# Optimization experiments

Hardware: AMD Instinct MI355X
Metric: run time of the kernel (lower is better)

Reference implementation:

```python
import jax, jax.numpy as jnp
import numpy as np

B, N, D = 64, 256, 768
ITER_STEPS = 1


def _linear_w(key, out_d, in_d):
    s = 1.0 / np.sqrt(in_d)
    return jax.random.uniform(key, (out_d, in_d), jnp.float32, -s, s)


def setup_inputs() -> dict:
    key = jax.random.key(0)
    ks = jax.random.split(key, 16)
    node = jax.random.normal(ks[0], (B, N, D), jnp.float32)
    node_mask = jnp.ones((B, N), jnp.int32)
    argument_graph = jax.random.randint(ks[1], (B, N, N), 0, 2, jnp.int32)
    punctuation_graph = jax.random.randint(ks[2], (B, N, N), 0, 2, jnp.int32)
    inp = {
        "node": node,
        "node_mask": node_mask,
        "argument_graph": argument_graph,
        "punctuation_graph": punctuation_graph,
        # node-relatedness scorer: Linear(D, 1, bias=True)
        "Wq": _linear_w(ks[3], 1, D),
        "bq": jnp.zeros((1,), jnp.float32),
        # self node fc: Linear(D, D, bias=True)
        "Ws": _linear_w(ks[4], D, D),
        "bs": jnp.zeros((D,), jnp.float32),
        # 8 relation projections, Linear(D, D, bias=False)
        "Wa": _linear_w(ks[5], D, D),
        "Wp": _linear_w(ks[6], D, D),
        "Wap": _linear_w(ks[7], D, D),
        "Wpp": _linear_w(ks[8], D, D),
        "Wa2": _linear_w(ks[9], D, D),
        "Wp2": _linear_w(ks[10], D, D),
        "Wap2": _linear_w(ks[11], D, D),
        "Wpp2": _linear_w(ks[12], D, D),
    }
    return inp


def reference(node, node_mask, argument_graph, punctuation_graph,
              Wq, bq, Ws, bs, Wa, Wp, Wap, Wpp, Wa2, Wp2, Wap2, Wpp2):
    f32 = jnp.float32
    mask = node_mask.astype(f32)                      # [B, N]
    n = node.shape[1]
    eye = jnp.eye(n, dtype=f32)
    # dd_graph: node_mask outer product with zeroed diagonal
    dd = mask[:, None, :] * mask[:, :, None] * (1.0 - eye)   # [B, N, N]
    g_a = dd * argument_graph.astype(f32)
    g_p = dd * punctuation_graph.astype(f32)
    # reverse directed edges
    g_ar = dd * jnp.swapaxes(g_a, 1, 2)
    g_pr = dd * jnp.swapaxes(g_p, 1, 2)
    neigh = g_a.sum(-1) + g_p.sum(-1) + g_ar.sum(-1) + g_pr.sum(-1)  # [B, N]
    denom = jnp.where(neigh >= 1.0, neigh, 1.0)

    all_weight = []
    for _ in range(ITER_STEPS):
        # (1) node relatedness
        dw = jax.nn.sigmoid(jnp.einsum('bnd,od->bno', node, Wq) + bq)[..., 0]  # [B, N]
        all_weight.append(dw)
        self_info = jnp.einsum('bnd,ed->bne', node, Ws) + bs

        def msg(g, W):
            # node_weight: broadcast dw over rows, zero where no edge
            nw = dw[:, None, :] * g                    # [B, N, N]
            proj = jnp.einsum('bnd,ed->bne', node, W)  # [B, N, D]
            return jnp.matmul(nw, proj)                # [B, N, D]

        agg = (msg(g_a, Wa) + msg(g_p, Wp) + msg(g_ar, Wap) + msg(g_pr, Wpp)
               + msg(g_a, Wa2) + msg(g_p, Wp2) + msg(g_ar, Wap2) + msg(g_pr, Wpp2))
        agg = agg / denom[..., None]
        # (3) node update
        node = jax.nn.relu(self_info + agg)

    all_weight = jnp.stack(all_weight, axis=1)  # [B, steps, N]
    return node, all_weight
```

## Files before the change

kernel.cpp:

```cpp
#include <hip/hip_runtime.h>
#include <hip/hip_bf16.h>
#include <math.h>

typedef __bf16 bf16;
typedef unsigned char u8;
typedef unsigned long long ull;
typedef __bf16 bf16x8 __attribute__((ext_vector_type(8)));
typedef float f32x4 __attribute__((ext_vector_type(4)));

#define BB 64
#define NN 256
#define DD 768
#define MM (BB*NN)
#define KP 1024
#define WSZ (DD*DD)
#define TL2 272
#define AROW2 196608


__device__ __forceinline__ void async16(const void* g, void* l) {
  __builtin_amdgcn_global_load_lds((__attribute__((address_space(1))) void*)g,
                                   (__attribute__((address_space(3))) void*)l,
                                   16, 0, 0);
}

__device__ __forceinline__ void stage_tile(const bf16* gsrc, int ld, char* ldst,
                                           int wv, int lane) {
#pragma unroll
  for (int cc = 0; cc < 2; ++cc) {
    int c = wv * 2 + cc;
    int row = c * 16 + (lane >> 2);
    int col = (lane & 3) * 8;
    async16(gsrc + (size_t)row * ld + col, ldst + c * 1024);
  }
}

__device__ __forceinline__ void mma_step(const char* lA, const char* lB,
                                         f32x4 acc[4][4], int lane, int wr, int wc) {
  bf16x8 af[4], bfr[4];
  int rbase = wr * 64 + (lane & 15);
  int cbase = wc * 64 + (lane & 15);
  int ko = (lane >> 4) * 8;
#pragma unroll
  for (int r = 0; r < 4; ++r)
    af[r] = *(const bf16x8*)(lA + (((rbase + r * 16) * 32) + ko) * 2);
#pragma unroll
  for (int c = 0; c < 4; ++c)
    bfr[c] = *(const bf16x8*)(lB + (((cbase + c * 16) * 32) + ko) * 2);
#pragma unroll
  for (int r = 0; r < 4; ++r)
#pragma unroll
    for (int c = 0; c < 4; ++c)
      acc[r][c] = __builtin_amdgcn_mfma_f32_16x16x32_bf16(af[r], bfr[c], acc[r][c], 0, 0, 0);
}

__device__ __forceinline__ void mma_step_fp8t(const char* lA, const char* lB,
                                              f32x4 acc[4][4], int lane, int wr, int wc) {
  long af[4], bfr[4];
  int koq = (lane >> 4) * 1024;
  int mA = (wr * 64 + (lane & 15)) * 8;
  int mB = (wc * 64 + (lane & 15)) * 8;
#pragma unroll
  for (int r = 0; r < 4; ++r)
    af[r] = *(const long*)(lA + koq + mA + r * 128);
#pragma unroll
  for (int c = 0; c < 4; ++c)
    bfr[c] = *(const long*)(lB + koq + mB + c * 128);
#pragma unroll
  for (int r = 0; r < 4; ++r)
#pragma unroll
    for (int c = 0; c < 4; ++c)
      acc[r][c] = __builtin_amdgcn_mfma_f32_16x16x32_fp8_fp8(af[r], bfr[c], acc[r][c], 0, 0, 0);
}

__device__ __forceinline__ void k_step64(const bf16* Ab, int lda, const bf16* Bb, int ldb,
                                         char* smem, f32x4 acc[4][4],
                                         int wv, int lane, int wr, int wc) {
  char* lA0 = smem;
  char* lA1 = smem + 8192;
  char* lB0 = smem + 16384;
  char* lB1 = smem + 24576;
  __syncthreads();
  stage_tile(Ab, lda, lA0, wv, lane);
  stage_tile(Ab + 32, lda, lA1, wv, lane);
  stage_tile(Bb, ldb, lB0, wv, lane);
  stage_tile(Bb + 32, ldb, lB1, wv, lane);
  __builtin_amdgcn_s_waitcnt(0);
  __syncthreads();
  mma_step(lA0, lB0, acc, lane, wr, wc);
  mma_step(lA1, lB1, acc, lane, wr, wc);
}

__device__ __forceinline__ unsigned pack4(float a, float b, float c, float d) {
  int w = 0;
  w = __builtin_amdgcn_cvt_pk_fp8_f32(a, b, w, false);
  w = __builtin_amdgcn_cvt_pk_fp8_f32(c, d, w, true);
  return (unsigned)w;
}

__global__ void k_pre(const float* __restrict__ node, const float* __restrict__ Wq,
                      const float* __restrict__ bq, bf16* __restrict__ node_bf,
                      float* __restrict__ dw, float* __restrict__ allw,
                      float* __restrict__ neigh,
                      const float* __restrict__ Ws,
                      const float* __restrict__ Wa, const float* __restrict__ Wp,
                      const float* __restrict__ Wap, const float* __restrict__ Wpp,
                      const float* __restrict__ Wa2, const float* __restrict__ Wp2,
                      const float* __restrict__ Wap2, const float* __restrict__ Wpp2,
                      bf16* __restrict__ Wcat4, bf16* __restrict__ Ws_bf) {
  if (blockIdx.x < MM / 4) {
    int lane = threadIdx.x & 63, wv = threadIdx.x >> 6;
    int row = blockIdx.x * 4 + wv;
    const float* nr = node + (size_t)row * DD;
    bf16* nb = node_bf + (size_t)row * DD;
    float s = 0.f;
#pragma unroll
    for (int k = 0; k < DD / 64; ++k) {
      int idx = lane + k * 64;
      float v = nr[idx];
      nb[idx] = (bf16)v;
      s += v * Wq[idx];
    }
#pragma unroll
    for (int off = 32; off; off >>= 1) s += __shfl_down(s, off);
    if (lane == 0) {
      float z = s + bq[0];
      float d = 1.f / (1.f + expf(-z));
      dw[row] = d;
      allw[row] = d;
      neigh[row] = 0.f;
    }
  } else {
    int i = (blockIdx.x - MM / 4) * 256 + threadIdx.x;
    Ws_bf[i] = (bf16)Ws[i];
    Wcat4[i]           = (bf16)(Wa[i] + Wa2[i]);
    Wcat4[i + WSZ]     = (bf16)(Wp[i] + Wp2[i]);
    Wcat4[i + 2 * WSZ] = (bf16)(Wap[i] + Wap2[i]);
    Wcat4[i + 3 * WSZ] = (bf16)(Wpp[i] + Wpp2[i]);
  }
}

__device__ __forceinline__ void store_tiled(u8* base, int tile, int kin, int m, uint4 v) {
  size_t o = (size_t)tile * 4096 + (size_t)((kin >> 3) * 1024 + m * 8);
  *(ull*)(base + o)        = ((ull)v.y << 32) | v.x;
  *(ull*)(base + o + 1024) = ((ull)v.w << 32) | v.z;
}

__global__ void k_graph(const int* __restrict__ mask, const int* __restrict__ arg,
                        const int* __restrict__ pun, const float* __restrict__ dw,
                        u8* __restrict__ g8, float* __restrict__ neigh) {
  __shared__ float la[64][65];
  __shared__ float lp[64][65];
  __shared__ float msk[256];
  __shared__ float dwv[256];
  int tid = threadIdx.x;
  int bi = blockIdx.x;
  int b = bi >> 4, it = (bi >> 2) & 3, jt = bi & 3;
  int i0 = it * 64, j0 = jt * 64;
  msk[tid] = (float)mask[b * NN + tid];
  dwv[tid] = dw[b * NN + tid];
  __syncthreads();
  int ir = tid >> 2, c4 = (tid & 3) * 16;
  int i = i0 + ir;
  float mi = msk[i];
  size_t gb = (size_t)b * NN * NN;
  const int* ap = arg + gb + (size_t)i * NN + j0 + c4;
  const int* pp = pun + gb + (size_t)i * NN + j0 + c4;
  float va[16], vp[16];
  float racc = 0.f;
#pragma unroll
  for (int k = 0; k < 16; ++k) {
    int j = j0 + c4 + k;
    float dd = (i == j) ? 0.f : mi * msk[j];
    float ga = dd * (float)ap[k];
    float gp = dd * (float)pp[k];
    la[ir][c4 + k] = ga;
    lp[ir][c4 + k] = gp;
    float w = dwv[j];
    va[k] = w * ga;
    vp[k] = w * gp;
    racc += ga + gp;
  }
  uint4 oa, op;
#pragma unroll
  for (int g = 0; g < 4; ++g) {
    (&oa.x)[g] = pack4(va[g*4], va[g*4+1], va[g*4+2], va[g*4+3]);
    (&op.x)[g] = pack4(vp[g*4], vp[g*4+1], vp[g*4+2], vp[g*4+3]);
  }
  {
    int tR = (b * 2 + (i >> 7)) * 32;
    int K0 = j0 + c4;
    store_tiled(g8, tR + (K0 >> 5),       K0 & 31, i & 127, oa);
    store_tiled(g8, tR + 8 + (K0 >> 5),   K0 & 31, i & 127, op);
  }
  racc += __shfl_xor(racc, 1);
  racc += __shfl_xor(racc, 2);
  if ((tid & 3) == 0) atomicAdd(&neigh[b * NN + i], racc);
  __syncthreads();
  int jr = ir, ic4 = c4;
  float cacc = 0.f;
#pragma unroll
  for (int k = 0; k < 16; ++k) {
    float ga = la[ic4 + k][jr];
    float gp = lp[ic4 + k][jr];
    float w = dwv[i0 + ic4 + k];
    va[k] = w * ga;
    vp[k] = w * gp;
    cacc += ga + gp;
  }
#pragma unroll
  for (int g = 0; g < 4; ++g) {
    (&oa.x)[g] = pack4(va[g*4], va[g*4+1], va[g*4+2], va[g*4+3]);
    (&op.x)[g] = pack4(vp[g*4], vp[g*4+1], vp[g*4+2], vp[g*4+3]);
  }
  {
    int row = j0 + jr;
    int tR = (b * 2 + (row >> 7)) * 32;
    int K2 = i0 + ic4;
    store_tiled(g8, tR + 16 + (K2 >> 5),  K2 & 31, row & 127, oa);
    store_tiled(g8, tR + 24 + (K2 >> 5),  K2 & 31, row & 127, op);
  }
  cacc += __shfl_xor(cacc, 1);
  cacc += __shfl_xor(cacc, 2);
  if ((tid & 3) == 0) atomicAdd(&neigh[b * NN + j0 + jr], cacc);
}

template<int VM>
__device__ __forceinline__ void wait_vm() {
  if constexpr (VM == 12)     asm volatile("s_waitcnt vmcnt(12)" ::: "memory");
  else if constexpr (VM == 8) asm volatile("s_waitcnt vmcnt(8)"  ::: "memory");
  else if constexpr (VM == 4) asm volatile("s_waitcnt vmcnt(4)"  ::: "memory");
  else                        asm volatile("s_waitcnt vmcnt(0)"  ::: "memory");
}

template<int P, int VM, bool STAGE>
__device__ __forceinline__ void proj_phase(int t, char* smem, int wvoff,
                                           const char* gA, const char* gB,
                                           int aoff, int boff, f32x4 (&acc)[8][4]) {
  if constexpr (STAGE) {
    int u = t + 3;
    char* D = smem + ((P + 3) & 3) * 32768 + wvoff;
    const char* sA = gA + u * 64;
    const char* sB = gB + u * 64;
    async16(sA,         D);
    async16(sA + AROW2, D + 8192);
    async16(sB,         D + 16384);
    async16(sB + AROW2, D + 24576);
  }
  wait_vm<VM>();
  __builtin_amdgcn_s_barrier();
  __builtin_amdgcn_sched_barrier(0);
  const char* L = smem + P * 32768;
  bf16x8 af[8], bfr[4];
#pragma unroll
  for (int r = 0; r < 8; ++r) af[r] = *(const bf16x8*)(L + aoff + r * 1024);
#pragma unroll
  for (int c = 0; c < 4; ++c) bfr[c] = *(const bf16x8*)(L + boff + c * 1024);
  __builtin_amdgcn_s_setprio(1);
#pragma unroll
  for (int r = 0; r < 8; ++r)
#pragma unroll
    for (int c = 0; c < 4; ++c)
      acc[r][c] = __builtin_amdgcn_mfma_f32_16x16x32_bf16(af[r], bfr[c], acc[r][c], 0, 0, 0);
  __builtin_amdgcn_s_setprio(0);
  __builtin_amdgcn_sched_barrier(0);
  __builtin_amdgcn_s_barrier();
}

__global__ __launch_bounds__(512, 2) void k_proj(const bf16* __restrict__ node_bf,
                                                 const bf16* __restrict__ Wcat4,
                                                 u8* __restrict__ p8) {
  __shared__ __align__(16) char smem[131072];
  int tid = threadIdx.x, lane = tid & 63, wv = tid >> 6;
  int wr = wv >> 2, wc = wv & 3;
  int l = blockIdx.x, xcd = l & 7, idx = l >> 3;
  int b = (idx / 12) * 8 + xcd;
  int nt = idx % 12;
  int n0 = nt * 256;
  int m0 = b * 256;
  int srcS = (tid & 3) ^ ((tid >> 3) & 3);
  const char* gA = (const char*)node_bf + (size_t)m0 * 1536 + (tid >> 2) * 1536 + srcS * 16;
  const char* gB = (const char*)Wcat4  + (size_t)n0 * 1536 + (tid >> 2) * 1536 + srcS * 16;
  int wvoff = wv * 1024;
  int sSwR = ((lane >> 4) ^ (((lane & 15) >> 1) & 3)) << 4;
  int aoff = (wr * 128 + (lane & 15)) * 64 + sSwR;
  int boff = 16384 + (wc * 64 + (lane & 15)) * 64 + sSwR;
  f32x4 z = {0.f, 0.f, 0.f, 0.f};
  f32x4 acc[8][4];
#pragma unroll
  for (int r = 0; r < 8; ++r)
#pragma unroll
    for (int c = 0; c < 4; ++c) acc[r][c] = z;
#pragma unroll
  for (int u = 0; u < 3; ++u) {
    char* D = smem + u * 32768 + wvoff;
    const char* sA = gA + u * 64;
    const char* sB = gB + u * 64;
    async16(sA,         D);
    async16(sA + AROW2, D + 8192);
    async16(sB,         D + 16384);
    async16(sB + AROW2, D + 24576);
  }
  for (int tt = 0; tt < 20; tt += 4) {
    proj_phase<0, 12, true>(tt + 0, smem, wvoff, gA, gB, aoff, boff, acc);
    proj_phase<1, 12, true>(tt + 1, smem, wvoff, gA, gB, aoff, boff, acc);
    proj_phase<2, 12, true>(tt + 2, smem, wvoff, gA, gB, aoff, boff, acc);
    proj_phase<3, 12, true>(tt + 3, smem, wvoff, gA, gB, aoff, boff, acc);
  }
  proj_phase<0, 12, true >(20, smem, wvoff, gA, gB, aoff, boff, acc);
  proj_phase<1,  8, false>(21, smem, wvoff, gA, gB, aoff, boff, acc);
  proj_phase<2,  4, false>(22, smem, wvoff, gA, gB, aoff, boff, acc);
  proj_phase<3,  0, false>(23, smem, wvoff, gA, gB, aoff, boff, acc);
  __syncthreads();
  u8* tb = (u8*)smem;
  int X = n0 / DD, e0 = n0 % DD;
#pragma unroll
  for (int r = 0; r < 8; ++r)
#pragma unroll
    for (int c = 0; c < 4; ++c) {
      int n = wc * 64 + c * 16 + (lane & 15);
      int m = wr * 128 + r * 16 + ((lane >> 4) << 2);
      *(unsigned*)(tb + n * TL2 + m) =
          pack4(acc[r][c][0], acc[r][c][1], acc[r][c][2], acc[r][c][3]);
    }
  __syncthreads();
#pragma unroll
  for (int t2 = 0; t2 < 8; ++t2) {
    int erow = t2 * 32 + (tid & 31);
    int col = (tid >> 5) * 16;
    uint4 v = *(const uint4*)(tb + erow * TL2 + col);
    int e = e0 + erow;
    int tR = (b * 6 + (e >> 7)) * 32 + X * 8;
    store_tiled(p8, tR + (col >> 5), col & 31, e & 127, v);
  }
}

__global__ __launch_bounds__(256) void k_agg(const u8* __restrict__ g8,
                                             const u8* __restrict__ p8,
                                             const bf16* __restrict__ node_bf,
                                             const bf16* __restrict__ Ws_bf,
                                             const float* __restrict__ neigh,
                                             const float* __restrict__ bs,
                                             float* __restrict__ out) {
  __shared__ __align__(16) char smem[32768];
  int tid = threadIdx.x, lane = tid & 63, wv = tid >> 6, wr = wv >> 1, wc = wv & 1;
  int l = blockIdx.x;
  int xcd = l & 7, idx = l >> 3;
  int b = (idx / 12) * 8 + xcd;
  int t = idx % 12;
  int i0 = (t / 6) * 128, e0 = (t % 6) * 128;
  f32x4 z = {0.f, 0.f, 0.f, 0.f};
  f32x4 acc[4][4];
#pragma unroll
  for (int r = 0; r < 4; ++r)
#pragma unroll
    for (int c = 0; c < 4; ++c) acc[r][c] = z;
  const u8* At = g8 + (size_t)((b * 2 + (i0 >> 7)) * 32) * 4096;
  const u8* Bt = p8 + (size_t)((b * 6 + (e0 >> 7)) * 32) * 4096;
  int lsoff = wv * 1024;
  int goff = lsoff + lane * 16;
  for (int k0 = 0; k0 < KP; k0 += 128) {
    __syncthreads();
#pragma unroll
    for (int s = 0; s < 4; ++s) {
      size_t toff = (size_t)((k0 >> 5) + s) * 4096 + goff;
      async16(At + toff, smem + s * 4096 + lsoff);
      async16(Bt + toff, smem + 16384 + s * 4096 + lsoff);
    }
    __builtin_amdgcn_s_waitcnt(0);
    __syncthreads();
#pragma unroll
    for (int s = 0; s < 4; ++s)
      mma_step_fp8t(smem + s * 4096, smem + 16384 + s * 4096, acc, lane, wr, wc);
  }
  int rowb = i0 + wr * 64 + (lane >> 4) * 4;
#pragma unroll
  for (int r = 0; r < 4; ++r)
#pragma unroll
    for (int q = 0; q < 4; ++q) {
      float rd = 1.f / fmaxf(neigh[b * NN + rowb + r * 16 + q], 1.f);
#pragma unroll
      for (int c = 0; c < 4; ++c) acc[r][c][q] *= rd;
    }
  const bf16* Ab2 = node_bf + (size_t)(b * NN + i0) * DD;
  const bf16* Bb2 = Ws_bf + (size_t)e0 * DD;
  for (int k0 = 0; k0 < DD; k0 += 64)
    k_step64(Ab2 + k0, DD, Bb2 + k0, DD, smem, acc, wv, lane, wr, wc);
  int colb = e0 + wc * 64 + (lane & 15);
#pragma unroll
  for (int c = 0; c < 4; ++c) {
    int col = colb + c * 16;
    float bv = bs[col];
#pragma unroll
    for (int r = 0; r < 4; ++r)
#pragma unroll
      for (int q = 0; q < 4; ++q) {
        int m = b * NN + rowb + r * 16 + q;
        out[(size_t)m * DD + col] = fmaxf(acc[r][c][q] + bv, 0.f);
      }
  }
}

extern "C" void kernel_launch(void* const* d_in, const int* in_sizes, int n_in,
                              void* d_out, int out_size, void* d_ws, size_t ws_size,
                              hipStream_t stream) {
  const float* node = (const float*)d_in[0];
  const int* mask   = (const int*)d_in[1];
  const int* arg    = (const int*)d_in[2];
  const int* pun    = (const int*)d_in[3];
  const float* Wq   = (const float*)d_in[4];
  const float* bq   = (const float*)d_in[5];
  const float* Ws   = (const float*)d_in[6];
  const float* bs   = (const float*)d_in[7];
  const float* Wa   = (const float*)d_in[8];
  const float* Wp   = (const float*)d_in[9];
  const float* Wap  = (const float*)d_in[10];
  const float* Wpp  = (const float*)d_in[11];
  const float* Wa2  = (const float*)d_in[12];
  const float* Wp2  = (const float*)d_in[13];
  const float* Wap2 = (const float*)d_in[14];
  const float* Wpp2 = (const float*)d_in[15];

  float* out  = (float*)d_out;
  float* allw = out + (size_t)MM * DD;

  char* ws = (char*)d_ws;
  bf16* node_bf = (bf16*)ws;
  float* dw     = (float*)(ws + 25165824);
  float* neigh  = (float*)(ws + 25231360);
  bf16* Wcat4   = (bf16*)(ws + 25296896);
  bf16* Ws_bf   = (bf16*)(ws + 30015488);
  u8*   g8      = (u8*)(ws + 31195136);
  u8*   p8      = (u8*)(ws + 47972352);
  (void)ws_size; (void)in_sizes; (void)n_in; (void)out_size;

  k_pre<<<MM / 4 + WSZ / 256, 256, 0, stream>>>(node, Wq, bq, node_bf, dw, allw,
                                                neigh, Ws, Wa, Wp, Wap, Wpp,
                                                Wa2, Wp2, Wap2, Wpp2, Wcat4, Ws_bf);
  k_graph<<<BB * 16, 256, 0, stream>>>(mask, arg, pun, dw, g8, neigh);
  k_proj<<<768, 512, 0, stream>>>(node_bf, Wcat4, p8);
  k_agg<<<12 * BB, 256, 0, stream>>>(g8, p8, node_bf, Ws_bf, neigh, bs, out);
}
```

Baseline: 319.6 us.

## Double-buffer LDS fragments in projection GEMM to overlap reads with MFMA

Restructures the k_proj main loop so that LDS fragment reads for the next k-step go into a second register set while MFMAs run on the current fragments. The global-to-LDS prefetch now goes four stages deep and is issued after the barrier, which drops the trailing barrier in each phase. The aim is to hide LDS read latency behind matrix-core work and cut per-iteration barrier stalls. The cost is higher register pressure from the doubled fragment buffers, which could spill or reduce occupancy at 2 blocks per CU, and the full unroll grows code size.

```diff
diff --git a/kernel.cpp b/kernel.cpp
--- a/kernel.cpp
+++ b/kernel.cpp
@@ -225,46 +225,43 @@
   if ((tid & 3) == 0) atomicAdd(&neigh[b * NN + j0 + jr], cacc);
 }
 
-template<int VM>
-__device__ __forceinline__ void wait_vm() {
-  if constexpr (VM == 12)     asm volatile("s_waitcnt vmcnt(12)" ::: "memory");
-  else if constexpr (VM == 8) asm volatile("s_waitcnt vmcnt(8)"  ::: "memory");
-  else if constexpr (VM == 4) asm volatile("s_waitcnt vmcnt(4)"  ::: "memory");
-  else                        asm volatile("s_waitcnt vmcnt(0)"  ::: "memory");
-}
-
-template<int P, int VM, bool STAGE>
-__device__ __forceinline__ void proj_phase(int t, char* smem, int wvoff,
-                                           const char* gA, const char* gB,
-                                           int aoff, int boff, f32x4 (&acc)[8][4]) {
-  if constexpr (STAGE) {
-    int u = t + 3;
-    char* D = smem + ((P + 3) & 3) * 32768 + wvoff;
-    const char* sA = gA + u * 64;
-    const char* sB = gB + u * 64;
+template<int T>
+__device__ __forceinline__ void proj_ph(char* smem, int wvoff,
+                                        const char* gA, const char* gB,
+                                        int aoff, int boff,
+                                        bf16x8 (&ca)[8], bf16x8 (&cb)[4],
+                                        bf16x8 (&na)[8], bf16x8 (&nb)[4],
+                                        f32x4 (&acc)[8][4]) {
+  if constexpr (T <= 20)      asm volatile("s_waitcnt vmcnt(8)" ::: "memory");
+  else if constexpr (T == 21) asm volatile("s_waitcnt vmcnt(4)" ::: "memory");
+  else                        asm volatile("s_waitcnt vmcnt(0)" ::: "memory");
+  __builtin_amdgcn_s_barrier();
+  __builtin_amdgcn_sched_barrier(0);
+  if constexpr (T + 4 < 24) {
+    char* D = smem + (T & 3) * 32768 + wvoff;
+    const char* sA = gA + (T + 4) * 64;
+    const char* sB = gB + (T + 4) * 64;
     async16(sA,         D);
     async16(sA + AROW2, D + 8192);
     async16(sB,         D + 16384);
     async16(sB + AROW2, D + 24576);
   }
-  wait_vm<VM>();
-  __builtin_amdgcn_s_barrier();
+  if constexpr (T + 1 < 24) {
+    const char* L = smem + ((T + 1) & 3) * 32768;
+#pragma unroll
+    for (int r = 0; r < 8; ++r) na[r] = *(const bf16x8*)(L + aoff + r * 1024);
+#pragma unroll
+    for (int c = 0; c < 4; ++c) nb[c] = *(const bf16x8*)(L + boff + c * 1024);
+  }
+  __builtin_amdgcn_s_setprio(1);
+#pragma unroll
+  for (int r = 0; r < 8; ++r)
+#pragma unroll
+    for (int c = 0; c < 4; ++c)
+      acc[r][c] = __builtin_amdgcn_mfma_f32_16x16x32_bf16(ca[r], cb[c], acc[r][c], 0, 0, 0);
+  __builtin_amdgcn_s_setprio(0);
+  asm volatile("s_waitcnt lgkmcnt(0)" ::: "memory");
   __builtin_amdgcn_sched_barrier(0);
-  const char* L = smem + P * 32768;
-  bf16x8 af[8], bfr[4];
-#pragma unroll
-  for (int r = 0; r < 8; ++r) af[r] = *(const bf16x8*)(L + aoff + r * 1024);
-#pragma unroll
-  for (int c = 0; c < 4; ++c) bfr[c] = *(const bf16x8*)(L + boff + c * 1024);
-  __builtin_amdgcn_s_setprio(1);
-#pragma unroll
-  for (int r = 0; r < 8; ++r)
-#pragma unroll
-    for (int c = 0; c < 4; ++c)
-      acc[r][c] = __builtin_amdgcn_mfma_f32_16x16x32_bf16(af[r], bfr[c], acc[r][c], 0, 0, 0);
-  __builtin_amdgcn_s_setprio(0);
-  __builtin_amdgcn_sched_barrier(0);
-  __builtin_amdgcn_s_barrier();
 }
 
 __global__ __launch_bounds__(512, 2) void k_proj(const bf16* __restrict__ node_bf,
@@ -291,8 +288,9 @@
   for (int r = 0; r < 8; ++r)
 #pragma unroll
     for (int c = 0; c < 4; ++c) acc[r][c] = z;
-#pragma unroll
-  for (int u = 0; u < 3; ++u) {
+  bf16x8 fa0[8], fb0[4], fa1[8], fb1[4];
+#pragma unroll
+  for (int u = 0; u < 4; ++u) {
     char* D = smem + u * 32768 + wvoff;
     const char* sA = gA + u * 64;
     const char* sB = gB + u * 64;
@@ -301,16 +299,39 @@
     async16(sB,         D + 16384);
     async16(sB + AROW2, D + 24576);
   }
-  for (int tt = 0; tt < 20; tt += 4) {
-    proj_phase<0, 12, true>(tt + 0, smem, wvoff, gA, gB, aoff, boff, acc);
-    proj_phase<1, 12, true>(tt + 1, smem, wvoff, gA, gB, aoff, boff, acc);
-    proj_phase<2, 12, true>(tt + 2, smem, wvoff, gA, gB, aoff, boff, acc);
-    proj_phase<3, 12, true>(tt + 3, smem, wvoff, gA, gB, aoff, boff, acc);
-  }
-  proj_phase<0, 12, true >(20, smem, wvoff, gA, gB, aoff, boff, acc);
-  proj_phase<1,  8, false>(21, smem, wvoff, gA, gB, aoff, boff, acc);
-  proj_phase<2,  4, false>(22, smem, wvoff, gA, gB, aoff, boff, acc);
-  proj_phase<3,  0, false>(23, smem, wvoff, gA, gB, aoff, boff, acc);
+  asm volatile("s_waitcnt vmcnt(12)" ::: "memory");
+  __builtin_amdgcn_s_barrier();
+  __builtin_amdgcn_sched_barrier(0);
+#pragma unroll
+  for (int r = 0; r < 8; ++r) fa0[r] = *(const bf16x8*)(smem + aoff + r * 1024);
+#pragma unroll
+  for (int c = 0; c < 4; ++c) fb0[c] = *(const bf16x8*)(smem + boff + c * 1024);
+  asm volatile("s_waitcnt lgkmcnt(0)" ::: "memory");
+  __builtin_amdgcn_sched_barrier(0);
+  proj_ph< 0>(smem, wvoff, gA, gB, aoff, boff, fa0, fb0, fa1, fb1, acc);
+  proj_ph< 1>(smem, wvoff, gA, gB, aoff, boff, fa1, fb1, fa0, fb0, acc);
+  proj_ph< 2>(smem, wvoff, gA, gB, aoff, boff, fa0, fb0, fa1, fb1, acc);
+  proj_ph< 3>(smem, wvoff, gA, gB, aoff, boff, fa1, fb1, fa0, fb0, acc);
+  proj_ph< 4>(smem, wvoff, gA, gB, aoff, boff, fa0, fb0, fa1, fb1, acc);
+  proj_ph< 5>(smem, wvoff, gA, gB, aoff, boff, fa1, fb1, fa0, fb0, acc);
+  proj_ph< 6>(smem, wvoff, gA, gB, aoff, boff, fa0, fb0, fa1, fb1, acc);
+  proj_ph< 7>(smem, wvoff, gA, gB, aoff, boff, fa1, fb1, fa0, fb0, acc);
+  proj_ph< 8>(smem, wvoff, gA, gB, aoff, boff, fa0, fb0, fa1, fb1, acc);
+  proj_ph< 9>(smem, wvoff, gA, gB, aoff, boff, fa1, fb1, fa0, fb0, acc);
+  proj_ph<10>(smem, wvoff, gA, gB, aoff, boff, fa0, fb0, fa1, fb1, acc);
+  proj_ph<11>(smem, wvoff, gA, gB, aoff, boff, fa1, fb1, fa0, fb0, acc);
+  proj_ph<12>(smem, wvoff, gA, gB, aoff, boff, fa0, fb0, fa1, fb1, acc);
+  proj_ph<13>(smem, wvoff, gA, gB, aoff, boff, fa1, fb1, fa0, fb0, acc);
+  proj_ph<14>(smem, wvoff, gA, gB, aoff, boff, fa0, fb0, fa1, fb1, acc);
+  proj_ph<15>(smem, wvoff, gA, gB, aoff, boff, fa1, fb1, fa0, fb0, acc);
+  proj_ph<16>(smem, wvoff, gA, gB, aoff, boff, fa0, fb0, fa1, fb1, acc);
+  proj_ph<17>(smem, wvoff, gA, gB, aoff, boff, fa1, fb1, fa0, fb0, acc);
+  proj_ph<18>(smem, wvoff, gA, gB, aoff, boff, fa0, fb0, fa1, fb1, acc);
+  proj_ph<19>(smem, wvoff, gA, gB, aoff, boff, fa1, fb1, fa0, fb0, acc);
+  proj_ph<20>(smem, wvoff, gA, gB, aoff, boff, fa0, fb0, fa1, fb1, acc);
+  proj_ph<21>(smem, wvoff, gA, gB, aoff, boff, fa1, fb1, fa0, fb0, acc);
+  proj_ph<22>(smem, wvoff, gA, gB, aoff, boff, fa0, fb0, fa1, fb1, acc);
+  proj_ph<23>(smem, wvoff, gA, gB, aoff, boff, fa1, fb1, fa0, fb0, acc);
   __syncthreads();
   u8* tb = (u8*)smem;
   int X = n0 / DD, e0 = n0 % DD;
```

After: 324.9 us. No clear change (+1.6%).
